# Optimization experiments

Measured on AMD Instinct MI355X. Metric: run time of the kernel, lower is better.

## Reference

```python
import jax, jax.numpy as jnp
import numpy as np

N = 16384
F = 256
RATIO = 0.5
K_KEEP = int(RATIO * N)  # 8192 nodes kept


def setup_inputs() -> dict:
    key = jax.random.key(0)
    k1, k2, k3 = jax.random.split(key, 3)
    X = jax.random.normal(k1, (N, F), dtype=jnp.float32)
    # binary-ish dense adjacency
    A = (jax.random.uniform(k2, (N, N), dtype=jnp.float32) < 0.01).astype(jnp.float32)
    p = jax.random.normal(k3, (F, 1), dtype=jnp.float32)
    return {"X": X, "A": A, "p": p}


def reference(X, A, p):
    # y = X p / ||p||  (scores), shape [N, 1]
    p_hat = p / jnp.sqrt(jnp.sum(p * p))
    y = X @ p_hat
    # global top-k (single-graph mode: I == zeros), indices sorted ascending
    _, idx = jax.lax.top_k(y[:, 0], K_KEEP)
    idx = jnp.sort(idx)
    # gated features, then gather kept nodes
    features = X * jnp.tanh(y)
    X_pooled = jnp.take(features, idx, axis=0)          # [K, F]
    # adjacency submatrix A[idx, idx]
    A_pooled = jnp.take(jnp.take(A, idx, axis=0), idx, axis=1)  # [K, K]
    return X_pooled, A_pooled
```

## Files before the change

kernel.cpp:

```cpp
#include <hip/hip_runtime.h>
#include <math.h>

#define N 16384
#define F 256
#define K_KEEP 8192
#define QS 4096
#define APOOL_BLOCKS (K_KEEP * 4)

typedef float f32x4 __attribute__((ext_vector_type(4)));

__global__ __launch_bounds__(256) void score_kernel(const float* __restrict__ X,
                                                    const float* __restrict__ p,
                                                    float* __restrict__ y) {
    const int wave = threadIdx.x >> 6;
    const int lane = threadIdx.x & 63;
    const int row  = blockIdx.x * 4 + wave;

    const float4 pv = *reinterpret_cast<const float4*>(p + lane * 4);
    const float4 xv = *reinterpret_cast<const float4*>(X + (size_t)row * F + lane * 4);

    double pp = (double)pv.x * pv.x + (double)pv.y * pv.y +
                (double)pv.z * pv.z + (double)pv.w * pv.w;
    double xp = (double)xv.x * pv.x + (double)xv.y * pv.y +
                (double)xv.z * pv.z + (double)xv.w * pv.w;

    #pragma unroll
    for (int off = 32; off >= 1; off >>= 1) {
        pp += __shfl_down(pp, off, 64);
        xp += __shfl_down(xp, off, 64);
    }
    if (lane == 0) y[row] = (float)(xp / sqrt(pp));
}

__global__ __launch_bounds__(1024) void select_emit_kernel(const float* __restrict__ y,
                                                           int* __restrict__ idx,
                                                           unsigned short* __restrict__ srcq,
                                                           int* __restrict__ wexcl) {
    __shared__ int hist[4096];
    __shared__ int part[1024];
    __shared__ int sc[256];
    __shared__ int bres[2];
    __shared__ float cand[1024];
    __shared__ int ccnt;
    __shared__ float sthr;
    __shared__ unsigned short fbw16[1024];
    const int t = threadIdx.x;

    #pragma unroll
    for (int q = 0; q < 4; ++q) hist[q * 1024 + t] = 0;
    if (t == 0) ccnt = 0;
    __syncthreads();

    float yv[16];
    const float4* __restrict__ y4 = reinterpret_cast<const float4*>(y + t * 16);
    #pragma unroll
    for (int q = 0; q < 4; ++q) {
        const float4 v = y4[q];
        yv[q * 4 + 0] = v.x; yv[q * 4 + 1] = v.y;
        yv[q * 4 + 2] = v.z; yv[q * 4 + 3] = v.w;
    }
    int bins[16];
    #pragma unroll
    for (int j = 0; j < 16; ++j) {
        const float v = fminf(fmaxf(yv[j] * 341.3333f + 2048.0f, 0.0f), 4095.0f);
        bins[j] = (int)v;
        atomicAdd(&hist[bins[j]], 1);
    }
    __syncthreads();

    part[t] = hist[t * 4] + hist[t * 4 + 1] + hist[t * 4 + 2] + hist[t * 4 + 3];
    __syncthreads();
    for (int off = 1; off < 1024; off <<= 1) {
        const int v = (t >= off) ? part[t - off] : 0;
        __syncthreads();
        part[t] += v;
        __syncthreads();
    }
    int acc = part[1023] - part[t];
    int fbin = -1, fr = 0;
    #pragma unroll
    for (int q = 3; q >= 0; --q) {
        const int b = t * 4 + q;
        const int h = hist[b];
        if (fbin < 0 && acc <= K_KEEP - 1 && K_KEEP - 1 < acc + h) {
            fbin = b; fr = K_KEEP - acc;
        }
        acc += h;
    }
    if (fbin >= 0) { bres[0] = fbin; bres[1] = fr; }
    __syncthreads();
    const int bstar = bres[0];
    const int r     = bres[1];

    #pragma unroll
    for (int j = 0; j < 16; ++j) {
        if (bins[j] == bstar) {
            const int pos = atomicAdd(&ccnt, 1);
            if (pos < 1024) cand[pos] = yv[j];
        }
    }
    __syncthreads();
    const int cc = (ccnt < 1024) ? ccnt : 1024;
    if (t < cc) {
        const float kk = cand[t];
        int g = 0;
        for (int j = 0; j < cc; ++j) g += (int)(cand[j] > kk);
        if (g == r - 1) sthr = kk;
    }
    __syncthreads();
    const float thr = sthr;

    unsigned int mask = 0;
    #pragma unroll
    for (int j = 0; j < 16; ++j) mask |= ((unsigned int)(yv[j] >= thr)) << j;
    fbw16[t] = (unsigned short)mask;
    __syncthreads();

    unsigned long long m = 0;
    if (t < 256) {
        m = (unsigned long long)fbw16[4 * t]
          | ((unsigned long long)fbw16[4 * t + 1] << 16)
          | ((unsigned long long)fbw16[4 * t + 2] << 32)
          | ((unsigned long long)fbw16[4 * t + 3] << 48);
        sc[t] = __popcll(m);
    }
    __syncthreads();
    for (int off = 1; off < 256; off <<= 1) {
        const int v = (t >= off && t < 256) ? sc[t - off] : 0;
        __syncthreads();
        if (t < 256) sc[t] += v;
        __syncthreads();
    }
    if (t < 256) {
        const int c = __popcll(m);
        int base = sc[t] - c;
        wexcl[t] = base;
        unsigned long long mm = m;
        const int col = t * 64;
        while (mm) {
            const int b = __ffsll((long long)mm) - 1;
            mm &= (mm - 1);
            const int i = col + b;
            idx[base]  = i;
            srcq[base] = (unsigned short)(i & (QS - 1));
            ++base;
        }
    }
}

__global__ __launch_bounds__(256) void pool_kernel(const float* __restrict__ A,
                                                   const float* __restrict__ X,
                                                   const float* __restrict__ y,
                                                   const int* __restrict__ idx,
                                                   const unsigned short* __restrict__ srcq,
                                                   const int* __restrict__ wexcl,
                                                   float* __restrict__ outX,
                                                   float* __restrict__ outA) {
    const int t = threadIdx.x;

    if (blockIdx.x >= APOOL_BLOCKS) {
        const int k    = (blockIdx.x - APOOL_BLOCKS) * 4 + (t >> 6);
        const int lane = t & 63;
        const int src  = idx[k];
        const float tf = tanhf(y[src]);
        const float4 xv = *reinterpret_cast<const float4*>(X + (size_t)src * F + lane * 4);
        float4 o = {xv.x * tf, xv.y * tf, xv.z * tf, xv.w * tf};
        *reinterpret_cast<float4*>(outX + (size_t)k * F + lane * 4) = o;
        return;
    }

    __shared__ float buf[QS];
    const int row  = blockIdx.x >> 2;
    const int h    = blockIdx.x & 3;
    const int ridx = idx[row];
    const int kb   = wexcl[h * 64];
    const int ke   = (h < 3) ? wexcl[h * 64 + 64] : K_KEEP;

    const f32x4* __restrict__ a4 =
        reinterpret_cast<const f32x4*>(A + (size_t)ridx * N + h * QS);
    f32x4* __restrict__ b4 = reinterpret_cast<f32x4*>(buf);
    #pragma unroll
    for (int s = 0; s < 4; ++s) b4[s * 256 + t] = __builtin_nontemporal_load(a4 + s * 256 + t);
    __syncthreads();

    float* __restrict__ orow = outA + (size_t)row * K_KEEP;
    const int k4b = (kb + 3) & ~3;
    const int k4e = ke & ~3;
    if (t < (k4b - kb)) orow[kb + t] = buf[srcq[kb + t]];
    if (t < (ke - k4e)) orow[k4e + t] = buf[srcq[k4e + t]];
    for (int k4 = k4b + 4 * t; k4 < k4e; k4 += 1024) {
        const ushort4 s4 = *reinterpret_cast<const ushort4*>(srcq + k4);
        f32x4 v = {buf[s4.x], buf[s4.y], buf[s4.z], buf[s4.w]};
        __builtin_nontemporal_store(v, reinterpret_cast<f32x4*>(orow + k4));
    }
}

extern "C" void kernel_launch(void* const* d_in, const int* in_sizes, int n_in,
                              void* d_out, int out_size, void* d_ws, size_t ws_size,
                              hipStream_t stream) {
    const float* X = (const float*)d_in[0];
    const float* A = (const float*)d_in[1];
    const float* p = (const float*)d_in[2];

    float* out  = (float*)d_out;
    float* outX = out;
    float* outA = out + (size_t)K_KEEP * F;

    char* ws = (char*)d_ws;
    float*          y     = (float*)ws;
    int*            wexcl = (int*)(ws + 65536);
    int*            idx   = (int*)(ws + 66560);
    unsigned short* srcq  = (unsigned short*)(ws + 99328);

    score_kernel<<<N / 4, 256, 0, stream>>>(X, p, y);
    select_emit_kernel<<<1, 1024, 0, stream>>>(y, idx, srcq, wexcl);
    pool_kernel<<<APOOL_BLOCKS + K_KEEP / 4, 256, 0, stream>>>(A, X, y, idx, srcq, wexcl,
                                                               outX, outA);
}
```

Before: 160.7 us.

## Replace dense adjacency gather with memset plus sparse nonzero scatter

Instead of staging quarter rows of A in shared memory and gathering the kept columns, the output adjacency is zeroed with a memset. Each kept row is then streamed once, and only its nonzero entries are scattered to their rank via a per-column rank table. This removes the shared-memory staging and the dense gather. It adds a separate full memset pass over the output and scattered single-float stores. It also normalises a negative zero in A to a positive zero.

```diff
diff --git a/kernel.cpp b/kernel.cpp
--- a/kernel.cpp
+++ b/kernel.cpp
@@ -4,8 +4,6 @@
 #define N 16384
 #define F 256
 #define K_KEEP 8192
-#define QS 4096
-#define APOOL_BLOCKS (K_KEEP * 4)
 
 typedef float f32x4 __attribute__((ext_vector_type(4)));
 
@@ -34,8 +32,7 @@
 
 __global__ __launch_bounds__(1024) void select_emit_kernel(const float* __restrict__ y,
                                                            int* __restrict__ idx,
-                                                           unsigned short* __restrict__ srcq,
-                                                           int* __restrict__ wexcl) {
+                                                           unsigned short* __restrict__ colrank) {
     __shared__ int hist[4096];
     __shared__ int part[1024];
     __shared__ int sc[256];
@@ -132,34 +129,31 @@
         __syncthreads();
     }
     if (t < 256) {
-        const int c = __popcll(m);
-        int base = sc[t] - c;
-        wexcl[t] = base;
-        unsigned long long mm = m;
+        int base = sc[t] - __popcll(m);
         const int col = t * 64;
-        while (mm) {
-            const int b = __ffsll((long long)mm) - 1;
-            mm &= (mm - 1);
-            const int i = col + b;
-            idx[base]  = i;
-            srcq[base] = (unsigned short)(i & (QS - 1));
-            ++base;
-        }
-    }
-}
-
-__global__ __launch_bounds__(256) void pool_kernel(const float* __restrict__ A,
-                                                   const float* __restrict__ X,
-                                                   const float* __restrict__ y,
-                                                   const int* __restrict__ idx,
-                                                   const unsigned short* __restrict__ srcq,
-                                                   const int* __restrict__ wexcl,
-                                                   float* __restrict__ outX,
-                                                   float* __restrict__ outA) {
+        for (int b = 0; b < 64; ++b) {
+            if ((m >> b) & 1ull) {
+                idx[base] = col + b;
+                colrank[col + b] = (unsigned short)base;
+                ++base;
+            } else {
+                colrank[col + b] = 0xFFFFu;
+            }
+        }
+    }
+}
+
+__global__ __launch_bounds__(256) void scatter_kernel(const float* __restrict__ A,
+                                                      const float* __restrict__ X,
+                                                      const float* __restrict__ y,
+                                                      const int* __restrict__ idx,
+                                                      const unsigned short* __restrict__ colrank,
+                                                      float* __restrict__ outX,
+                                                      float* __restrict__ outA) {
     const int t = threadIdx.x;
 
-    if (blockIdx.x >= APOOL_BLOCKS) {
-        const int k    = (blockIdx.x - APOOL_BLOCKS) * 4 + (t >> 6);
+    if (blockIdx.x >= K_KEEP) {
+        const int k    = (blockIdx.x - K_KEEP) * 4 + (t >> 6);
         const int lane = t & 63;
         const int src  = idx[k];
         const float tf = tanhf(y[src]);
@@ -169,29 +163,27 @@
         return;
     }
 
-    __shared__ float buf[QS];
-    const int row  = blockIdx.x >> 2;
-    const int h    = blockIdx.x & 3;
+    const int row  = blockIdx.x;
     const int ridx = idx[row];
-    const int kb   = wexcl[h * 64];
-    const int ke   = (h < 3) ? wexcl[h * 64 + 64] : K_KEEP;
-
-    const f32x4* __restrict__ a4 =
-        reinterpret_cast<const f32x4*>(A + (size_t)ridx * N + h * QS);
-    f32x4* __restrict__ b4 = reinterpret_cast<f32x4*>(buf);
-    #pragma unroll
-    for (int s = 0; s < 4; ++s) b4[s * 256 + t] = __builtin_nontemporal_load(a4 + s * 256 + t);
-    __syncthreads();
-
+    const float* __restrict__ arow = A + (size_t)ridx * N;
     float* __restrict__ orow = outA + (size_t)row * K_KEEP;
-    const int k4b = (kb + 3) & ~3;
-    const int k4e = ke & ~3;
-    if (t < (k4b - kb)) orow[kb + t] = buf[srcq[kb + t]];
-    if (t < (ke - k4e)) orow[k4e + t] = buf[srcq[k4e + t]];
-    for (int k4 = k4b + 4 * t; k4 < k4e; k4 += 1024) {
-        const ushort4 s4 = *reinterpret_cast<const ushort4*>(srcq + k4);
-        f32x4 v = {buf[s4.x], buf[s4.y], buf[s4.z], buf[s4.w]};
-        __builtin_nontemporal_store(v, reinterpret_cast<f32x4*>(orow + k4));
+
+    #pragma unroll 4
+    for (int it = 0; it < 16; ++it) {
+        const int c0 = it * 1024 + t * 4;
+        const f32x4 v = __builtin_nontemporal_load(
+            reinterpret_cast<const f32x4*>(arow + c0));
+        if (v.x != 0.0f || v.y != 0.0f || v.z != 0.0f || v.w != 0.0f) {
+            #pragma unroll
+            for (int e = 0; e < 4; ++e) {
+                const float ve = v[e];
+                if (ve != 0.0f) {
+                    const unsigned short cr = colrank[c0 + e];
+                    if (cr != 0xFFFFu)
+                        __builtin_nontemporal_store(ve, orow + cr);
+                }
+            }
+        }
     }
 }
 
@@ -207,13 +199,13 @@
     float* outA = out + (size_t)K_KEEP * F;
 
     char* ws = (char*)d_ws;
-    float*          y     = (float*)ws;
-    int*            wexcl = (int*)(ws + 65536);
-    int*            idx   = (int*)(ws + 66560);
-    unsigned short* srcq  = (unsigned short*)(ws + 99328);
-
+    float*          y       = (float*)ws;
+    int*            idx     = (int*)(ws + 65536);
+    unsigned short* colrank = (unsigned short*)(ws + 98304);
+
+    hipMemsetAsync(outA, 0, (size_t)K_KEEP * K_KEEP * sizeof(float), stream);
     score_kernel<<<N / 4, 256, 0, stream>>>(X, p, y);
-    select_emit_kernel<<<1, 1024, 0, stream>>>(y, idx, srcq, wexcl);
-    pool_kernel<<<APOOL_BLOCKS + K_KEEP / 4, 256, 0, stream>>>(A, X, y, idx, srcq, wexcl,
-                                                               outX, outA);
-}
+    select_emit_kernel<<<1, 1024, 0, stream>>>(y, idx, colrank);
+    scatter_kernel<<<K_KEEP + K_KEEP / 4, 256, 0, stream>>>(A, X, y, idx, colrank,
+                                                            outX, outA);
+}
```

After: 210.5 us. 1.31x slower.
